# Performance work log

Measured on AMD Instinct MI355X. Metric: run time of the kernel, lower is better.

## Reference

```python
import jax, jax.numpy as jnp
import numpy as np

TEMP = 0.07


def setup_inputs() -> dict:
    key = jax.random.key(0)
    k1, k2 = jax.random.split(key)
    N, C = 8192, 512
    X = jax.random.normal(k1, (N, C), dtype=jnp.float32)
    Y = jax.random.normal(k2, (N, C), dtype=jnp.float32)
    return {"X": X, "Y": Y}


def reference(X, Y):
    # Original loop computes, per row i, cross-entropy over logits
    # [X_i.Y_i, X_i.Y_j (j != i)] / temp with label 0 (the positive).
    # Softmax CE is permutation-invariant, so this equals
    #   logsumexp(S_i / temp) - S_ii / temp,  S = X @ Y^T,
    # summed over rows (loop accumulates with +=, i.e. sum reduction).
    S = jnp.einsum('nc,mc->nm', X, Y) / TEMP  # [N, N]
    lse = jax.nn.logsumexp(S, axis=1)          # [N]
    pos = jnp.diagonal(S)                      # [N]
    return jnp.sum(lse - pos)
```

## Files before the change

kernel.cpp:

```cpp
#include <hip/hip_runtime.h>
#include <stdint.h>

#define N 8192
#define C 512
#define BM 128
#define BN 128
#define BKF 128
#define NSPLIT 16
#define COLS_PER_SPLIT (N / NSPLIT)
#define CT (COLS_PER_SPLIT / BN)
#define INV_T 14.285714285714286f

typedef __attribute__((ext_vector_type(4)))  int   i32x4;
typedef __attribute__((ext_vector_type(8)))  int   i32x8;
typedef __attribute__((ext_vector_type(16))) float f32x16;

__global__ __launch_bounds__(256) void prep_kernel(const float* __restrict__ X,
                                                   const float* __restrict__ Y,
                                                   unsigned char* __restrict__ Xf8,
                                                   unsigned char* __restrict__ Yf8,
                                                   float* __restrict__ pos) {
  const int wave = threadIdx.x >> 6;
  const int lane = threadIdx.x & 63;
  const int row = blockIdx.x * 4 + wave;
  const float4* xr = (const float4*)(X + (size_t)row * C) + lane * 2;
  const float4* yr = (const float4*)(Y + (size_t)row * C) + lane * 2;
  float4 x0 = xr[0], x1 = xr[1];
  float4 y0 = yr[0], y1 = yr[1];
  float s = x0.x * y0.x + x0.y * y0.y + x0.z * y0.z + x0.w * y0.w
          + x1.x * y1.x + x1.y * y1.y + x1.z * y1.z + x1.w * y1.w;
  int2 ox, oy;
  ox.x = __builtin_amdgcn_cvt_pk_fp8_f32(x0.x, x0.y, 0, false);
  ox.x = __builtin_amdgcn_cvt_pk_fp8_f32(x0.z, x0.w, ox.x, true);
  ox.y = __builtin_amdgcn_cvt_pk_fp8_f32(x1.x, x1.y, 0, false);
  ox.y = __builtin_amdgcn_cvt_pk_fp8_f32(x1.z, x1.w, ox.y, true);
  oy.x = __builtin_amdgcn_cvt_pk_fp8_f32(y0.x, y0.y, 0, false);
  oy.x = __builtin_amdgcn_cvt_pk_fp8_f32(y0.z, y0.w, oy.x, true);
  oy.y = __builtin_amdgcn_cvt_pk_fp8_f32(y1.x, y1.y, 0, false);
  oy.y = __builtin_amdgcn_cvt_pk_fp8_f32(y1.z, y1.w, oy.y, true);
  ((int2*)(Xf8 + (size_t)row * C))[lane] = ox;
  ((int2*)(Yf8 + (size_t)row * C))[lane] = oy;
#pragma unroll
  for (int off = 32; off >= 1; off >>= 1) s += __shfl_xor(s, off);
  if (lane == 0) pos[row] = s * INV_T;
}

__global__ __launch_bounds__(256, 3) void gemm_lse_kernel(const unsigned char* __restrict__ Xf8,
                                                          const unsigned char* __restrict__ Yf8,
                                                          float2* __restrict__ partials) {
  __shared__ unsigned char As[BM][BKF];
  __shared__ unsigned char Bs[BN][BKF];

  const int tid = threadIdx.x;
  const int bx = blockIdx.x;
  const int split = bx & (NSPLIT - 1);
  const int rb = bx >> 4;
  const int row0 = rb * BM;
  const int colbase = split * COLS_PER_SPLIT;

  const int w = tid >> 6;
  const int lane = tid & 63;
  const int lrow = lane & 31;
  const int h = lane >> 5;
  const int arow = w * 32 + lrow;
  const int swz = lrow & 7;

  float m_s[16], l_s[16];
#pragma unroll
  for (int s = 0; s < 16; ++s) { m_s[s] = -INFINITY; l_s[s] = 0.0f; }

  const int r_base = tid >> 3;
  const int p = tid & 7;
  const int j = p ^ (r_base & 7);

  for (int ct = 0; ct < CT; ++ct) {
    const int col0 = colbase + ct * BN;
    f32x16 acc[4];
#pragma unroll
    for (int t = 0; t < 4; ++t)
#pragma unroll
      for (int e = 0; e < 16; ++e) acc[t][e] = 0.0f;

    for (int k0 = 0; k0 < C; k0 += BKF) {
#pragma unroll
      for (int i = 0; i < 4; ++i) {
        const int r = i * 32 + r_base;
        const unsigned char* ga = Xf8 + (size_t)(row0 + r) * C + (k0 + j * 16);
        const unsigned char* gb = Yf8 + (size_t)(col0 + r) * C + (k0 + j * 16);
        uint32_t loff = (uint32_t)((i * 256 + (tid & ~63)) * 16);
        __builtin_amdgcn_global_load_lds(
            (const __attribute__((address_space(1))) uint32_t*)(uintptr_t)ga,
            (__attribute__((address_space(3))) uint32_t*)(uintptr_t)((char*)&As[0][0] + loff),
            16, 0, 0);
        __builtin_amdgcn_global_load_lds(
            (const __attribute__((address_space(1))) uint32_t*)(uintptr_t)gb,
            (__attribute__((address_space(3))) uint32_t*)(uintptr_t)((char*)&Bs[0][0] + loff),
            16, 0, 0);
      }
      __syncthreads();
#pragma unroll
      for (int s = 0; s < 2; ++s) {
        const int c0 = 4 * s + 2 * h;
        i32x4 alo = *(const i32x4*)&As[arow][((c0    ) ^ swz) * 16];
        i32x4 ahi = *(const i32x4*)&As[arow][((c0 + 1) ^ swz) * 16];
        i32x8 af = { alo[0], alo[1], alo[2], alo[3], ahi[0], ahi[1], ahi[2], ahi[3] };
#pragma unroll
        for (int tj = 0; tj < 4; ++tj) {
          const int brow = tj * 32 + lrow;
          i32x4 blo = *(const i32x4*)&Bs[brow][((c0    ) ^ swz) * 16];
          i32x4 bhi = *(const i32x4*)&Bs[brow][((c0 + 1) ^ swz) * 16];
          i32x8 bf = { blo[0], blo[1], blo[2], blo[3], bhi[0], bhi[1], bhi[2], bhi[3] };
          acc[tj] = __builtin_amdgcn_mfma_scale_f32_32x32x64_f8f6f4(
              af, bf, acc[tj], 0, 0, 0, 127, 0, 127);
        }
      }
      __syncthreads();
    }

#pragma unroll
    for (int r = 0; r < 16; ++r) {
      float v0 = acc[0][r] * INV_T;
      float v1 = acc[1][r] * INV_T;
      float v2 = acc[2][r] * INV_T;
      float v3 = acc[3][r] * INV_T;
      float mx = fmaxf(fmaxf(v0, v1), fmaxf(v2, v3));
      float mn = fmaxf(m_s[r], mx);
      l_s[r] = l_s[r] * __expf(m_s[r] - mn)
             + __expf(v0 - mn) + __expf(v1 - mn) + __expf(v2 - mn) + __expf(v3 - mn);
      m_s[r] = mn;
    }
  }

#pragma unroll
  for (int r = 0; r < 16; ++r) {
    float m = m_s[r], l = l_s[r];
#pragma unroll
    for (int off = 1; off < 32; off <<= 1) {
      float mo = __shfl_xor(m, off);
      float lo = __shfl_xor(l, off);
      float mn = fmaxf(m, mo);
      l = l * __expf(m - mn) + lo * __expf(mo - mn);
      m = mn;
    }
    m_s[r] = m; l_s[r] = l;
  }
  if (lrow == 0) {
#pragma unroll
    for (int r = 0; r < 16; ++r) {
      int row_local = (r & 3) + 8 * (r >> 2) + 4 * h;
      partials[(size_t)(row0 + w * 32 + row_local) * NSPLIT + split] =
          make_float2(m_s[r], l_s[r]);
    }
  }
}

__global__ __launch_bounds__(256) void combine_kernel(const float2* __restrict__ partials,
                                                      const float* __restrict__ pos,
                                                      float* __restrict__ out) {
  int row = blockIdx.x * 256 + threadIdx.x;
  const float2* pr = partials + (size_t)row * NSPLIT;
  float M = -INFINITY;
  float2 p[NSPLIT];
#pragma unroll
  for (int s = 0; s < NSPLIT; ++s) { p[s] = pr[s]; M = fmaxf(M, p[s].x); }
  float L = 0.0f;
#pragma unroll
  for (int s = 0; s < NSPLIT; ++s) L += p[s].y * __expf(p[s].x - M);
  float v = M + __logf(L) - pos[row];
#pragma unroll
  for (int off = 32; off >= 1; off >>= 1) v += __shfl_xor(v, off);
  __shared__ float wsum[4];
  if ((threadIdx.x & 63) == 0) wsum[threadIdx.x >> 6] = v;
  __syncthreads();
  if (threadIdx.x == 0) atomicAdd(out, wsum[0] + wsum[1] + wsum[2] + wsum[3]);
}

extern "C" void kernel_launch(void* const* d_in, const int* in_sizes, int n_in,
                              void* d_out, int out_size, void* d_ws, size_t ws_size,
                              hipStream_t stream) {
  const float* X = (const float*)d_in[0];
  const float* Y = (const float*)d_in[1];
  float* out = (float*)d_out;

  char* w = (char*)d_ws;
  unsigned char* Xf8 = (unsigned char*)w;
  unsigned char* Yf8 = Xf8 + (size_t)N * C;
  float2* partials = (float2*)(Yf8 + (size_t)N * C);
  float* pos = (float*)((char*)partials + (size_t)N * NSPLIT * sizeof(float2));

  hipMemsetAsync(d_out, 0, sizeof(float), stream);
  prep_kernel<<<N / 4, 256, 0, stream>>>(X, Y, Xf8, Yf8, pos);
  gemm_lse_kernel<<<64 * NSPLIT, 256, 0, stream>>>(Xf8, Yf8, partials);
  combine_kernel<<<N / 256, 256, 0, stream>>>(partials, pos, out);
}
```

Baseline: 140.2 us.

## Fuse combine step into GEMM via last-block ticket and drop memset

Removes the separate combine kernel and the output memset. Each GEMM block takes a ticket from an atomic counter that the prep kernel resets, and the last block to finish merges all split partials, subtracts the positives and writes the final sum directly. The partials layout changes to split-major so the reduction reads are coalesced. This saves two launches and their gaps, but the final reduction over 8192 rows now runs serially in a single block at the tail.

```diff
diff --git a/kernel.cpp b/kernel.cpp
--- a/kernel.cpp
+++ b/kernel.cpp
@@ -9,6 +9,7 @@
 #define NSPLIT 16
 #define COLS_PER_SPLIT (N / NSPLIT)
 #define CT (COLS_PER_SPLIT / BN)
+#define GRID_GEMM (64 * NSPLIT)
 #define INV_T 14.285714285714286f
 
 typedef __attribute__((ext_vector_type(4)))  int   i32x4;
@@ -19,7 +20,9 @@
                                                    const float* __restrict__ Y,
                                                    unsigned char* __restrict__ Xf8,
                                                    unsigned char* __restrict__ Yf8,
-                                                   float* __restrict__ pos) {
+                                                   float* __restrict__ pos,
+                                                   unsigned* __restrict__ ticket) {
+  if (blockIdx.x == 0 && threadIdx.x == 0) *ticket = 0u;
   const int wave = threadIdx.x >> 6;
   const int lane = threadIdx.x & 63;
   const int row = blockIdx.x * 4 + wave;
@@ -47,7 +50,10 @@
 
 __global__ __launch_bounds__(256, 3) void gemm_lse_kernel(const unsigned char* __restrict__ Xf8,
                                                           const unsigned char* __restrict__ Yf8,
-                                                          float2* __restrict__ partials) {
+                                                          float2* __restrict__ partials,
+                                                          const float* __restrict__ pos,
+                                                          unsigned* __restrict__ ticket,
+                                                          float* __restrict__ out) {
   __shared__ unsigned char As[BM][BKF];
   __shared__ unsigned char Bs[BN][BKF];
 
@@ -148,31 +154,41 @@
 #pragma unroll
     for (int r = 0; r < 16; ++r) {
       int row_local = (r & 3) + 8 * (r >> 2) + 4 * h;
-      partials[(size_t)(row0 + w * 32 + row_local) * NSPLIT + split] =
+      partials[(size_t)split * N + (row0 + w * 32 + row_local)] =
           make_float2(m_s[r], l_s[r]);
     }
   }
-}
-
-__global__ __launch_bounds__(256) void combine_kernel(const float2* __restrict__ partials,
-                                                      const float* __restrict__ pos,
-                                                      float* __restrict__ out) {
-  int row = blockIdx.x * 256 + threadIdx.x;
-  const float2* pr = partials + (size_t)row * NSPLIT;
-  float M = -INFINITY;
-  float2 p[NSPLIT];
-#pragma unroll
-  for (int s = 0; s < NSPLIT; ++s) { p[s] = pr[s]; M = fmaxf(M, p[s].x); }
-  float L = 0.0f;
-#pragma unroll
-  for (int s = 0; s < NSPLIT; ++s) L += p[s].y * __expf(p[s].x - M);
-  float v = M + __logf(L) - pos[row];
-#pragma unroll
-  for (int off = 32; off >= 1; off >>= 1) v += __shfl_xor(v, off);
-  __shared__ float wsum[4];
-  if ((threadIdx.x & 63) == 0) wsum[threadIdx.x >> 6] = v;
+
   __syncthreads();
-  if (threadIdx.x == 0) atomicAdd(out, wsum[0] + wsum[1] + wsum[2] + wsum[3]);
+  __shared__ unsigned last;
+  if (tid == 0) {
+    __threadfence();
+    unsigned rank = __hip_atomic_fetch_add(ticket, 1u, __ATOMIC_ACQ_REL,
+                                           __HIP_MEMORY_SCOPE_AGENT);
+    last = (rank == GRID_GEMM - 1) ? 1u : 0u;
+  }
+  __syncthreads();
+  if (last) {
+    float v = 0.0f;
+    for (int k = 0; k < 32; ++k) {
+      const int row = tid + 256 * k;
+      float M = -INFINITY, L = 0.0f;
+#pragma unroll
+      for (int s = 0; s < NSPLIT; ++s) {
+        float2 pr = partials[(size_t)s * N + row];
+        float mn = fmaxf(M, pr.x);
+        L = L * __expf(M - mn) + pr.y * __expf(pr.x - mn);
+        M = mn;
+      }
+      v += M + __logf(L) - pos[row];
+    }
+#pragma unroll
+    for (int off = 32; off >= 1; off >>= 1) v += __shfl_xor(v, off);
+    __shared__ float wsum[4];
+    if ((tid & 63) == 0) wsum[tid >> 6] = v;
+    __syncthreads();
+    if (tid == 0) out[0] = wsum[0] + wsum[1] + wsum[2] + wsum[3];
+  }
 }
 
 extern "C" void kernel_launch(void* const* d_in, const int* in_sizes, int n_in,
@@ -186,10 +202,9 @@
   unsigned char* Xf8 = (unsigned char*)w;
   unsigned char* Yf8 = Xf8 + (size_t)N * C;
   float2* partials = (float2*)(Yf8 + (size_t)N * C);
-  float* pos = (float*)((char*)partials + (size_t)N * NSPLIT * sizeof(float2));
-
-  hipMemsetAsync(d_out, 0, sizeof(float), stream);
-  prep_kernel<<<N / 4, 256, 0, stream>>>(X, Y, Xf8, Yf8, pos);
-  gemm_lse_kernel<<<64 * NSPLIT, 256, 0, stream>>>(Xf8, Yf8, partials);
-  combine_kernel<<<N / 256, 256, 0, stream>>>(partials, pos, out);
+  float* pos = (float*)((char*)partials + (size_t)NSPLIT * N * sizeof(float2));
+  unsigned* ticket = (unsigned*)(pos + N);
+
+  prep_kernel<<<N / 4, 256, 0, stream>>>(X, Y, Xf8, Yf8, pos, ticket);
+  gemm_lse_kernel<<<GRID_GEMM, 256, 0, stream>>>(Xf8, Yf8, partials, pos, ticket, out);
 }
```

After: 203.6 us. 45.3% more time.

## Keep full-K X tile resident in LDS and halve column splits

Applied to the files above, without the earlier changes.

The GEMM kernel now loads the whole 128x512 FP8 X row block into shared memory once, instead of reloading it for every column tile and K step. Only Y tiles are streamed per step. The column split drops from 16 to 8, which halves the grid and doubles the column tiles per block, and launch bounds drop to 2 blocks per CU to fit the larger LDS footprint. The partials layout becomes split-major and the combine kernel uses an online max/sum merge. This trades occupancy and parallelism for less global and LDS traffic on X.

```diff
diff --git a/kernel.cpp b/kernel.cpp
--- a/kernel.cpp
+++ b/kernel.cpp
@@ -6,9 +6,10 @@
 #define BM 128
 #define BN 128
 #define BKF 128
-#define NSPLIT 16
+#define NSPLIT 8
 #define COLS_PER_SPLIT (N / NSPLIT)
 #define CT (COLS_PER_SPLIT / BN)
+#define GRID_GEMM (64 * NSPLIT)
 #define INV_T 14.285714285714286f
 
 typedef __attribute__((ext_vector_type(4)))  int   i32x4;
@@ -45,16 +46,16 @@
   if (lane == 0) pos[row] = s * INV_T;
 }
 
-__global__ __launch_bounds__(256, 3) void gemm_lse_kernel(const unsigned char* __restrict__ Xf8,
+__global__ __launch_bounds__(256, 2) void gemm_lse_kernel(const unsigned char* __restrict__ Xf8,
                                                           const unsigned char* __restrict__ Yf8,
                                                           float2* __restrict__ partials) {
-  __shared__ unsigned char As[BM][BKF];
+  __shared__ unsigned char As[BM][C];
   __shared__ unsigned char Bs[BN][BKF];
 
   const int tid = threadIdx.x;
   const int bx = blockIdx.x;
   const int split = bx & (NSPLIT - 1);
-  const int rb = bx >> 4;
+  const int rb = bx >> 3;
   const int row0 = rb * BM;
   const int colbase = split * COLS_PER_SPLIT;
 
@@ -65,6 +66,22 @@
   const int arow = w * 32 + lrow;
   const int swz = lrow & 7;
 
+#pragma unroll
+  for (int t = 0; t < 16; ++t) {
+    const int s2 = t * 256 + tid;
+    const int r = s2 >> 5;
+    const int cir = s2 & 31;
+    const int k0t = cir >> 3;
+    const int p = cir & 7;
+    const int jj = p ^ (r & 7);
+    const unsigned char* ga = Xf8 + (size_t)(row0 + r) * C + k0t * BKF + jj * 16;
+    uint32_t loff = (uint32_t)((t * 256 + (tid & ~63)) * 16);
+    __builtin_amdgcn_global_load_lds(
+        (const __attribute__((address_space(1))) uint32_t*)(uintptr_t)ga,
+        (__attribute__((address_space(3))) uint32_t*)(uintptr_t)((char*)&As[0][0] + loff),
+        16, 0, 0);
+  }
+
   float m_s[16], l_s[16];
 #pragma unroll
   for (int s = 0; s < 16; ++s) { m_s[s] = -INFINITY; l_s[s] = 0.0f; }
@@ -81,17 +98,12 @@
 #pragma unroll
       for (int e = 0; e < 16; ++e) acc[t][e] = 0.0f;
 
-    for (int k0 = 0; k0 < C; k0 += BKF) {
+    for (int k0 = 0; k0 < C / BKF; ++k0) {
 #pragma unroll
       for (int i = 0; i < 4; ++i) {
         const int r = i * 32 + r_base;
-        const unsigned char* ga = Xf8 + (size_t)(row0 + r) * C + (k0 + j * 16);
-        const unsigned char* gb = Yf8 + (size_t)(col0 + r) * C + (k0 + j * 16);
+        const unsigned char* gb = Yf8 + (size_t)(col0 + r) * C + k0 * BKF + j * 16;
         uint32_t loff = (uint32_t)((i * 256 + (tid & ~63)) * 16);
-        __builtin_amdgcn_global_load_lds(
-            (const __attribute__((address_space(1))) uint32_t*)(uintptr_t)ga,
-            (__attribute__((address_space(3))) uint32_t*)(uintptr_t)((char*)&As[0][0] + loff),
-            16, 0, 0);
         __builtin_amdgcn_global_load_lds(
             (const __attribute__((address_space(1))) uint32_t*)(uintptr_t)gb,
             (__attribute__((address_space(3))) uint32_t*)(uintptr_t)((char*)&Bs[0][0] + loff),
@@ -101,8 +113,8 @@
 #pragma unroll
       for (int s = 0; s < 2; ++s) {
         const int c0 = 4 * s + 2 * h;
-        i32x4 alo = *(const i32x4*)&As[arow][((c0    ) ^ swz) * 16];
-        i32x4 ahi = *(const i32x4*)&As[arow][((c0 + 1) ^ swz) * 16];
+        i32x4 alo = *(const i32x4*)&As[arow][k0 * BKF + (((c0    ) ^ swz) * 16)];
+        i32x4 ahi = *(const i32x4*)&As[arow][k0 * BKF + (((c0 + 1) ^ swz) * 16)];
         i32x8 af = { alo[0], alo[1], alo[2], alo[3], ahi[0], ahi[1], ahi[2], ahi[3] };
 #pragma unroll
         for (int tj = 0; tj < 4; ++tj) {
@@ -148,7 +160,7 @@
 #pragma unroll
     for (int r = 0; r < 16; ++r) {
       int row_local = (r & 3) + 8 * (r >> 2) + 4 * h;
-      partials[(size_t)(row0 + w * 32 + row_local) * NSPLIT + split] =
+      partials[(size_t)split * N + (row0 + w * 32 + row_local)] =
           make_float2(m_s[r], l_s[r]);
     }
   }
@@ -158,14 +170,14 @@
                                                       const float* __restrict__ pos,
                                                       float* __restrict__ out) {
   int row = blockIdx.x * 256 + threadIdx.x;
-  const float2* pr = partials + (size_t)row * NSPLIT;
-  float M = -INFINITY;
-  float2 p[NSPLIT];
-#pragma unroll
-  for (int s = 0; s < NSPLIT; ++s) { p[s] = pr[s]; M = fmaxf(M, p[s].x); }
-  float L = 0.0f;
-#pragma unroll
-  for (int s = 0; s < NSPLIT; ++s) L += p[s].y * __expf(p[s].x - M);
+  float M = -INFINITY, L = 0.0f;
+#pragma unroll
+  for (int s = 0; s < NSPLIT; ++s) {
+    float2 pr = partials[(size_t)s * N + row];
+    float mn = fmaxf(M, pr.x);
+    L = L * __expf(M - mn) + pr.y * __expf(pr.x - mn);
+    M = mn;
+  }
   float v = M + __logf(L) - pos[row];
 #pragma unroll
   for (int off = 32; off >= 1; off >>= 1) v += __shfl_xor(v, off);
@@ -186,10 +198,10 @@
   unsigned char* Xf8 = (unsigned char*)w;
   unsigned char* Yf8 = Xf8 + (size_t)N * C;
   float2* partials = (float2*)(Yf8 + (size_t)N * C);
-  float* pos = (float*)((char*)partials + (size_t)N * NSPLIT * sizeof(float2));
+  float* pos = (float*)((char*)partials + (size_t)NSPLIT * N * sizeof(float2));
 
   hipMemsetAsync(d_out, 0, sizeof(float), stream);
   prep_kernel<<<N / 4, 256, 0, stream>>>(X, Y, Xf8, Yf8, pos);
-  gemm_lse_kernel<<<64 * NSPLIT, 256, 0, stream>>>(Xf8, Yf8, partials);
+  gemm_lse_kernel<<<GRID_GEMM, 256, 0, stream>>>(Xf8, Yf8, partials);
   combine_kernel<<<N / 256, 256, 0, stream>>>(partials, pos, out);
 }
```

New measurement: 123.2 us. -12.1%, faster.
